# Performance work log

Hardware: AMD Instinct MI355X
Metric: run time of the kernel (lower is better)

## Reference

```python
import jax, jax.numpy as jnp
import numpy as np

H = 64          # hidden_dim
G = 4           # grid_size
NB = 4.0        # neighborhood
PRED = 12       # pred_steps


def _social_pool(all_h, positions, idx, W_sp, b_sp):
    """Vectorized grid-based social pooling. all_h:(N,H), positions:(N,2) -> (H,)."""
    N = positions.shape[0]
    pos_i = positions[idx]
    diff = positions - pos_i                                   # (N,2)
    in_nb = jnp.max(jnp.abs(diff), axis=1) <= NB
    mask = in_nb & (jnp.arange(N) != idx)
    # torch: int(clamp(((d/NB)+1)/2 * G, 0, G-1)); truncation==floor after clip here
    g = jnp.clip(jnp.floor((diff / NB + 1.0) / 2.0 * G), 0, G - 1).astype(jnp.int32)
    cell = g[:, 1] * G + g[:, 0]                               # gy*G + gx, (N,)
    m = mask.astype(all_h.dtype)[:, None]                      # (N,1)
    grid = jax.ops.segment_sum(all_h * m, cell, num_segments=G * G)   # (16,H)
    counts = jax.ops.segment_sum(m, cell, num_segments=G * G)         # (16,1)
    pooled = (grid / jnp.maximum(counts, 1.0)).sum(axis=0)            # (H,)
    return pooled @ W_sp.T + b_sp


def _lstm_cell(inp, h, c, W_ih, b_ih, W_hh, b_hh):
    gates = inp @ W_ih.T + b_ih + h @ W_hh.T + b_hh            # (4H,)
    i, f, g, o = jnp.split(gates, 4)
    i, f, o = jax.nn.sigmoid(i), jax.nn.sigmoid(f), jax.nn.sigmoid(o)
    g = jnp.tanh(g)
    c_new = f * c + i * g
    return o * jnp.tanh(c_new), c_new


def setup_inputs() -> dict:
    key = jax.random.key(0)
    ks = jax.random.split(key, 10)
    N, T = 2_000_000, 8
    s = 0.05
    return {
        "history": jax.random.normal(ks[0], (T, 4), jnp.float32),
        "all_h": jax.random.normal(ks[1], (N, H), jnp.float32),
        "positions": jax.random.normal(ks[2], (N, 2), jnp.float32) * 3.0,
        "W_in": jax.random.normal(ks[3], (H, 4), jnp.float32) * s,
        "b_in": jnp.zeros((H,), jnp.float32),
        "W_ih": jax.random.normal(ks[4], (4 * H, 2 * H), jnp.float32) * s,
        "b_ih": jnp.zeros((4 * H,), jnp.float32),
        "W_hh": jax.random.normal(ks[5], (4 * H, H), jnp.float32) * s,
        "b_hh": jnp.zeros((4 * H,), jnp.float32),
        "W_sp": jax.random.normal(ks[6], (H, H), jnp.float32) * s,
        "b_sp": jnp.zeros((H,), jnp.float32),
        "W_out": jax.random.normal(ks[7], (2, H), jnp.float32) * s,
        "b_out": jnp.zeros((2,), jnp.float32),
        "idx": 0,
    }


def reference(history, all_h, positions, W_in, b_in, W_ih, b_ih, W_hh, b_hh,
              W_sp, b_sp, W_out, b_out, idx):
    # all_h, positions, idx are fixed inputs, so the social vector is identical
    # at every timestep (same math as recomputing it each step in the original).
    social = _social_pool(all_h, positions, idx, W_sp, b_sp)   # (H,)

    def enc_step(carry, x):
        h, c = carry
        emb = x @ W_in.T + b_in
        inp = jnp.concatenate([emb, social])
        h, c = _lstm_cell(inp, h, c, W_ih, b_ih, W_hh, b_hh)
        return (h, c), None

    h0 = jnp.zeros((H,), history.dtype)
    (h, c), _ = jax.lax.scan(enc_step, (h0, h0), history)

    last_pos = history[-1, :2]

    def pred_step(carry, _):
        h, c, lp = carry
        delta = h @ W_out.T + b_out                            # (2,)
        vel = delta / 0.5
        x = jnp.concatenate([lp + delta, vel])                 # (4,)
        emb = x @ W_in.T + b_in
        inp = jnp.concatenate([emb, social])
        h, c = _lstm_cell(inp, h, c, W_ih, b_ih, W_hh, b_hh)
        return (h, c, lp + delta), delta

    _, preds = jax.lax.scan(pred_step, (h, c, last_pos), None, length=PRED)
    return preds  # (pred_steps, 2)
```

## Files before the change

kernel.cpp:

```cpp
#include <hip/hip_runtime.h>

#define HDIM 64
#define CELLS 16
#define WPB 4
#define PV (CELLS * HDIM + CELLS)

__global__ void __launch_bounds__(256) k_pool(
    const float* __restrict__ all_h, const float2* __restrict__ pos2,
    const int* __restrict__ idxp, float* __restrict__ partial,
    int N, int nwaves)
{
    __shared__ float acc[WPB][CELLS * HDIM];
    __shared__ float cnt[WPB][CELLS];
    __shared__ __align__(16) int lst[WPB][64];
    const int tid  = threadIdx.x;
    const int wave = tid >> 6;
    const int lane = tid & 63;

    for (int v = tid; v < WPB * CELLS * HDIM; v += 256) ((float*)acc)[v] = 0.0f;
    if (tid < WPB * CELLS) ((float*)cnt)[tid] = 0.0f;
    __syncthreads();

    const int    idx0 = idxp[0];
    const float2 p0   = pos2[idx0];
    const int    gw   = blockIdx.x * WPB + wave;
    float* __restrict__ accw = acc[wave];
    int*   __restrict__ lstw = lst[wave];

    for (int base = gw * 64; base < N; base += nwaves * 64) {
        const int a = base + lane;
        int cellid = -1;
        if (a < N && a != idx0) {
            const float2 p = pos2[a];
            const float dx = p.x - p0.x;
            const float dy = p.y - p0.y;
            if (fmaxf(fabsf(dx), fabsf(dy)) <= 4.0f) {
                const float f0 = floorf((dx / 4.0f + 1.0f) / 2.0f * 4.0f);
                const float f1 = floorf((dy / 4.0f + 1.0f) / 2.0f * 4.0f);
                const int g0 = (int)fminf(fmaxf(f0, 0.0f), 3.0f);
                const int g1 = (int)fminf(fmaxf(f1, 0.0f), 3.0f);
                cellid = g1 * 4 + g0;
                atomicAdd(&cnt[wave][cellid], 1.0f);
            }
        }
        const unsigned long long mask  = __ballot(cellid >= 0);
        const int                M     = __popcll(mask);
        const unsigned long long below = mask & ((1ULL << lane) - 1ULL);
        if (cellid >= 0) lstw[__popcll(below)] = (lane << 4) | cellid;

        const float* __restrict__ rowp = all_h + (size_t)base * HDIM + lane;
        int r = 0;
        for (; r + 8 <= M; r += 8) {
            const int4 e0 = *(const int4*)&lstw[r];
            const int4 e1 = *(const int4*)&lstw[r + 4];
            const float v0 = rowp[(size_t)(e0.x >> 4) * HDIM];
            const float v1 = rowp[(size_t)(e0.y >> 4) * HDIM];
            const float v2 = rowp[(size_t)(e0.z >> 4) * HDIM];
            const float v3 = rowp[(size_t)(e0.w >> 4) * HDIM];
            const float v4 = rowp[(size_t)(e1.x >> 4) * HDIM];
            const float v5 = rowp[(size_t)(e1.y >> 4) * HDIM];
            const float v6 = rowp[(size_t)(e1.z >> 4) * HDIM];
            const float v7 = rowp[(size_t)(e1.w >> 4) * HDIM];
            accw[(e0.x & 15) * HDIM + lane] += v0;
            accw[(e0.y & 15) * HDIM + lane] += v1;
            accw[(e0.z & 15) * HDIM + lane] += v2;
            accw[(e0.w & 15) * HDIM + lane] += v3;
            accw[(e1.x & 15) * HDIM + lane] += v4;
            accw[(e1.y & 15) * HDIM + lane] += v5;
            accw[(e1.z & 15) * HDIM + lane] += v6;
            accw[(e1.w & 15) * HDIM + lane] += v7;
        }
        for (; r < M; ++r) {
            const int e = lstw[r];
            accw[(e & 15) * HDIM + lane] += rowp[(size_t)(e >> 4) * HDIM];
        }
    }
    __syncthreads();

    float* __restrict__ outp = partial + (size_t)blockIdx.x * PV;
    for (int v = tid; v < CELLS * HDIM; v += 256)
        outp[v] = acc[0][v] + acc[1][v] + acc[2][v] + acc[3][v];
    if (tid < CELLS)
        outp[CELLS * HDIM + tid] = cnt[0][tid] + cnt[1][tid] + cnt[2][tid] + cnt[3][tid];
}

__global__ void __launch_bounds__(256) k_reduce(
    const float* __restrict__ partial, float* __restrict__ finalv, int nbp)
{
    const int wave = threadIdx.x >> 6;
    const int lane = threadIdx.x & 63;
    const int v = blockIdx.x * 4 + wave;
    if (v >= PV) return;
    float s = 0.0f;
    for (int b = lane; b < nbp; b += 64)
        s += partial[(size_t)b * PV + v];
    #pragma unroll
    for (int off = 32; off > 0; off >>= 1)
        s += __shfl_xor(s, off);
    if (lane == 0) finalv[v] = s;
}

__global__ void __launch_bounds__(256) k_lstm(
    const float* __restrict__ finalv, const float* __restrict__ history,
    const float* __restrict__ W_in, const float* __restrict__ b_in,
    const float* __restrict__ W_ih, const float* __restrict__ b_ih,
    const float* __restrict__ W_hh, const float* __restrict__ b_hh,
    const float* __restrict__ W_sp, const float* __restrict__ b_sp,
    const float* __restrict__ W_out, const float* __restrict__ b_out,
    float* __restrict__ out)
{
    __shared__ __align__(16) float pooled[64];
    __shared__ __align__(16) float social[64];
    __shared__ __align__(16) float hl[64];
    __shared__ __align__(16) float cl[64];
    __shared__ float gl[256];
    __shared__ float xs[4];
    __shared__ float lp[2];
    __shared__ float dl[2];
    const int tid = threadIdx.x;

    if (tid < 64) {
        float p = 0.0f;
        #pragma unroll
        for (int c = 0; c < CELLS; ++c) {
            const float cc = finalv[CELLS * HDIM + c];
            p += finalv[c * HDIM + tid] / fmaxf(cc, 1.0f);
        }
        pooled[tid] = p;
    }
    __syncthreads();
    if (tid < 64) {
        float s = b_sp[tid];
        for (int k = 0; k < 64; k += 4) {
            const float4 w4 = *(const float4*)&W_sp[tid * 64 + k];
            s += pooled[k] * w4.x + pooled[k + 1] * w4.y
               + pooled[k + 2] * w4.z + pooled[k + 3] * w4.w;
        }
        social[tid] = s;
        hl[tid] = 0.0f;
        cl[tid] = 0.0f;
    }
    if (tid < 2) lp[tid] = history[7 * 4 + tid];
    __syncthreads();

    float m1k[4] = {0.0f, 0.0f, 0.0f, 0.0f};
    float gconst = b_ih[tid] + b_hh[tid];
    for (int m = 0; m < 64; m += 4) {
        const float4 w4 = *(const float4*)&W_ih[tid * 128 + m];
        const float4 a0 = *(const float4*)&W_in[m * 4];
        const float4 a1 = *(const float4*)&W_in[(m + 1) * 4];
        const float4 a2 = *(const float4*)&W_in[(m + 2) * 4];
        const float4 a3 = *(const float4*)&W_in[(m + 3) * 4];
        m1k[0] += w4.x * a0.x + w4.y * a1.x + w4.z * a2.x + w4.w * a3.x;
        m1k[1] += w4.x * a0.y + w4.y * a1.y + w4.z * a2.y + w4.w * a3.y;
        m1k[2] += w4.x * a0.z + w4.y * a1.z + w4.z * a2.z + w4.w * a3.z;
        m1k[3] += w4.x * a0.w + w4.y * a1.w + w4.z * a2.w + w4.w * a3.w;
        gconst += w4.x * b_in[m] + w4.y * b_in[m + 1]
                + w4.z * b_in[m + 2] + w4.w * b_in[m + 3];
    }
    for (int k = 0; k < 64; k += 4) {
        const float4 w4 = *(const float4*)&W_ih[tid * 128 + 64 + k];
        gconst += w4.x * social[k] + w4.y * social[k + 1]
                + w4.z * social[k + 2] + w4.w * social[k + 3];
    }
    float whh[64];
    #pragma unroll
    for (int k = 0; k < 64; k += 4) {
        const float4 w4 = *(const float4*)&W_hh[tid * 64 + k];
        whh[k] = w4.x; whh[k + 1] = w4.y; whh[k + 2] = w4.z; whh[k + 3] = w4.w;
    }

    for (int t = 0; t < 8; ++t) {
        __syncthreads();
        if (tid < 4) xs[tid] = history[t * 4 + tid];
        __syncthreads();
        float g0 = gconst + m1k[0] * xs[0] + m1k[1] * xs[1];
        float g1 = m1k[2] * xs[2] + m1k[3] * xs[3];
        float g2 = 0.0f, g3 = 0.0f;
        #pragma unroll
        for (int k = 0; k < 64; k += 16) {
            const float4 a = *(const float4*)&hl[k];
            const float4 b = *(const float4*)&hl[k + 4];
            const float4 c = *(const float4*)&hl[k + 8];
            const float4 d = *(const float4*)&hl[k + 12];
            g0 += whh[k] * a.x + whh[k + 1] * a.y + whh[k + 2] * a.z + whh[k + 3] * a.w;
            g1 += whh[k + 4] * b.x + whh[k + 5] * b.y + whh[k + 6] * b.z + whh[k + 7] * b.w;
            g2 += whh[k + 8] * c.x + whh[k + 9] * c.y + whh[k + 10] * c.z + whh[k + 11] * c.w;
            g3 += whh[k + 12] * d.x + whh[k + 13] * d.y + whh[k + 14] * d.z + whh[k + 15] * d.w;
        }
        gl[tid] = (g0 + g1) + (g2 + g3);
        __syncthreads();
        if (tid < 64) {
            const float ig = 1.0f / (1.0f + expf(-gl[tid]));
            const float fg = 1.0f / (1.0f + expf(-gl[64 + tid]));
            const float gg = tanhf(gl[128 + tid]);
            const float og = 1.0f / (1.0f + expf(-gl[192 + tid]));
            const float cn = fg * cl[tid] + ig * gg;
            cl[tid] = cn;
            hl[tid] = og * tanhf(cn);
        }
    }

    for (int t = 0; t < 12; ++t) {
        __syncthreads();
        if (tid < 2) {
            float d = b_out[tid];
            for (int k = 0; k < 64; k += 4) {
                const float4 w4 = *(const float4*)&W_out[tid * 64 + k];
                d += w4.x * hl[k] + w4.y * hl[k + 1] + w4.z * hl[k + 2] + w4.w * hl[k + 3];
            }
            dl[tid] = d;
            out[t * 2 + tid] = d;
        }
        __syncthreads();
        if (tid < 2) {
            const float npos = lp[tid] + dl[tid];
            xs[tid] = npos;
            xs[2 + tid] = dl[tid] * 2.0f;
            lp[tid] = npos;
        }
        __syncthreads();
        float g0 = gconst + m1k[0] * xs[0] + m1k[1] * xs[1];
        float g1 = m1k[2] * xs[2] + m1k[3] * xs[3];
        float g2 = 0.0f, g3 = 0.0f;
        #pragma unroll
        for (int k = 0; k < 64; k += 16) {
            const float4 a = *(const float4*)&hl[k];
            const float4 b = *(const float4*)&hl[k + 4];
            const float4 c = *(const float4*)&hl[k + 8];
            const float4 d = *(const float4*)&hl[k + 12];
            g0 += whh[k] * a.x + whh[k + 1] * a.y + whh[k + 2] * a.z + whh[k + 3] * a.w;
            g1 += whh[k + 4] * b.x + whh[k + 5] * b.y + whh[k + 6] * b.z + whh[k + 7] * b.w;
            g2 += whh[k + 8] * c.x + whh[k + 9] * c.y + whh[k + 10] * c.z + whh[k + 11] * c.w;
            g3 += whh[k + 12] * d.x + whh[k + 13] * d.y + whh[k + 14] * d.z + whh[k + 15] * d.w;
        }
        gl[tid] = (g0 + g1) + (g2 + g3);
        __syncthreads();
        if (tid < 64) {
            const float ig = 1.0f / (1.0f + expf(-gl[tid]));
            const float fg = 1.0f / (1.0f + expf(-gl[64 + tid]));
            const float gg = tanhf(gl[128 + tid]);
            const float og = 1.0f / (1.0f + expf(-gl[192 + tid]));
            const float cn = fg * cl[tid] + ig * gg;
            cl[tid] = cn;
            hl[tid] = og * tanhf(cn);
        }
    }
}

extern "C" void kernel_launch(void* const* d_in, const int* in_sizes, int n_in,
                              void* d_out, int out_size, void* d_ws, size_t ws_size,
                              hipStream_t stream) {
    const float* history   = (const float*)d_in[0];
    const float* all_h     = (const float*)d_in[1];
    const float* positions = (const float*)d_in[2];
    const float* W_in  = (const float*)d_in[3];
    const float* b_in  = (const float*)d_in[4];
    const float* W_ih  = (const float*)d_in[5];
    const float* b_ih  = (const float*)d_in[6];
    const float* W_hh  = (const float*)d_in[7];
    const float* b_hh  = (const float*)d_in[8];
    const float* W_sp  = (const float*)d_in[9];
    const float* b_sp  = (const float*)d_in[10];
    const float* W_out = (const float*)d_in[11];
    const float* b_out = (const float*)d_in[12];
    const int*   idxp  = (const int*)d_in[13];
    const int N = in_sizes[2] / 2;

    float* ws      = (float*)d_ws;
    float* finalv  = ws;
    float* partial = ws + PV;

    long long avail = (long long)(ws_size / sizeof(float)) - PV;
    int nbp = 2048;
    if ((long long)nbp * PV > avail) nbp = (int)(avail / PV);
    if (nbp < 1) nbp = 1;

    k_pool<<<nbp, 256, 0, stream>>>(all_h, (const float2*)positions, idxp,
                                    partial, N, nbp * WPB);
    k_reduce<<<(PV + 3) / 4, 256, 0, stream>>>(partial, finalv, nbp);
    k_lstm<<<1, 256, 0, stream>>>(finalv, history, W_in, b_in, W_ih, b_ih,
                                  W_hh, b_hh, W_sp, b_sp, W_out, b_out,
                                  (float*)d_out);
}
```

Baseline: 75.75 us.

## Precompute LSTM input constants in reduce kernel, warm caches, trim LSTM syncs

An extra block is added to the reduce kernel. It precomputes the input-projection folding (W_ih times W_in, plus the bias constant) into workspace, and touches the W_ih, W_hh, W_sp and W_out weights to warm the cache ahead of the serial LSTM kernel. The LSTM kernel now caches history in shared memory and computes the output projection with a wave shuffle reduction instead of two threads. This removes two barriers per prediction step. The pooling gather loop also gains a 16-wide unrolled stage to raise memory-level parallelism, at the cost of more registers.

```diff
diff --git a/kernel.cpp b/kernel.cpp
--- a/kernel.cpp
+++ b/kernel.cpp
@@ -4,6 +4,11 @@
 #define CELLS 16
 #define WPB 4
 #define PV (CELLS * HDIM + CELLS)
+
+#define WS_M1K   1040
+#define WS_G0    2064
+#define WS_SINK  2320
+#define WS_PART  2576
 
 __global__ void __launch_bounds__(256) k_pool(
     const float* __restrict__ all_h, const float2* __restrict__ pos2,
@@ -50,6 +55,44 @@
 
         const float* __restrict__ rowp = all_h + (size_t)base * HDIM + lane;
         int r = 0;
+        for (; r + 16 <= M; r += 16) {
+            const int4 e0 = *(const int4*)&lstw[r];
+            const int4 e1 = *(const int4*)&lstw[r + 4];
+            const int4 e2 = *(const int4*)&lstw[r + 8];
+            const int4 e3 = *(const int4*)&lstw[r + 12];
+            const float v0  = rowp[(size_t)(e0.x >> 4) * HDIM];
+            const float v1  = rowp[(size_t)(e0.y >> 4) * HDIM];
+            const float v2  = rowp[(size_t)(e0.z >> 4) * HDIM];
+            const float v3  = rowp[(size_t)(e0.w >> 4) * HDIM];
+            const float v4  = rowp[(size_t)(e1.x >> 4) * HDIM];
+            const float v5  = rowp[(size_t)(e1.y >> 4) * HDIM];
+            const float v6  = rowp[(size_t)(e1.z >> 4) * HDIM];
+            const float v7  = rowp[(size_t)(e1.w >> 4) * HDIM];
+            const float v8  = rowp[(size_t)(e2.x >> 4) * HDIM];
+            const float v9  = rowp[(size_t)(e2.y >> 4) * HDIM];
+            const float v10 = rowp[(size_t)(e2.z >> 4) * HDIM];
+            const float v11 = rowp[(size_t)(e2.w >> 4) * HDIM];
+            const float v12 = rowp[(size_t)(e3.x >> 4) * HDIM];
+            const float v13 = rowp[(size_t)(e3.y >> 4) * HDIM];
+            const float v14 = rowp[(size_t)(e3.z >> 4) * HDIM];
+            const float v15 = rowp[(size_t)(e3.w >> 4) * HDIM];
+            accw[(e0.x & 15) * HDIM + lane] += v0;
+            accw[(e0.y & 15) * HDIM + lane] += v1;
+            accw[(e0.z & 15) * HDIM + lane] += v2;
+            accw[(e0.w & 15) * HDIM + lane] += v3;
+            accw[(e1.x & 15) * HDIM + lane] += v4;
+            accw[(e1.y & 15) * HDIM + lane] += v5;
+            accw[(e1.z & 15) * HDIM + lane] += v6;
+            accw[(e1.w & 15) * HDIM + lane] += v7;
+            accw[(e2.x & 15) * HDIM + lane] += v8;
+            accw[(e2.y & 15) * HDIM + lane] += v9;
+            accw[(e2.z & 15) * HDIM + lane] += v10;
+            accw[(e2.w & 15) * HDIM + lane] += v11;
+            accw[(e3.x & 15) * HDIM + lane] += v12;
+            accw[(e3.y & 15) * HDIM + lane] += v13;
+            accw[(e3.z & 15) * HDIM + lane] += v14;
+            accw[(e3.w & 15) * HDIM + lane] += v15;
+        }
         for (; r + 8 <= M; r += 8) {
             const int4 e0 = *(const int4*)&lstw[r];
             const int4 e1 = *(const int4*)&lstw[r + 4];
@@ -85,26 +128,63 @@
 }
 
 __global__ void __launch_bounds__(256) k_reduce(
-    const float* __restrict__ partial, float* __restrict__ finalv, int nbp)
-{
-    const int wave = threadIdx.x >> 6;
-    const int lane = threadIdx.x & 63;
-    const int v = blockIdx.x * 4 + wave;
-    if (v >= PV) return;
-    float s = 0.0f;
-    for (int b = lane; b < nbp; b += 64)
-        s += partial[(size_t)b * PV + v];
-    #pragma unroll
-    for (int off = 32; off > 0; off >>= 1)
-        s += __shfl_xor(s, off);
-    if (lane == 0) finalv[v] = s;
-}
-
-__global__ void __launch_bounds__(256) k_lstm(
-    const float* __restrict__ finalv, const float* __restrict__ history,
+    const float* __restrict__ partial, float* __restrict__ ws,
     const float* __restrict__ W_in, const float* __restrict__ b_in,
     const float* __restrict__ W_ih, const float* __restrict__ b_ih,
     const float* __restrict__ W_hh, const float* __restrict__ b_hh,
+    const float* __restrict__ W_sp, const float* __restrict__ W_out,
+    int nbp)
+{
+    const int tid = threadIdx.x;
+    if (blockIdx.x < 260) {
+        const int wave = tid >> 6;
+        const int lane = tid & 63;
+        const int v = blockIdx.x * 4 + wave;
+        if (v >= PV) return;
+        float s = 0.0f;
+        for (int b = lane; b < nbp; b += 64)
+            s += partial[(size_t)b * PV + v];
+        #pragma unroll
+        for (int off = 32; off > 0; off >>= 1)
+            s += __shfl_xor(s, off);
+        if (lane == 0) ws[v] = s;
+        return;
+    }
+    float m0 = 0.0f, m1 = 0.0f, m2 = 0.0f, m3 = 0.0f;
+    float gc = b_ih[tid] + b_hh[tid];
+    for (int m = 0; m < 64; m += 4) {
+        const float4 w4 = *(const float4*)&W_ih[tid * 128 + m];
+        const float4 a0 = *(const float4*)&W_in[m * 4];
+        const float4 a1 = *(const float4*)&W_in[(m + 1) * 4];
+        const float4 a2 = *(const float4*)&W_in[(m + 2) * 4];
+        const float4 a3 = *(const float4*)&W_in[(m + 3) * 4];
+        m0 += w4.x * a0.x + w4.y * a1.x + w4.z * a2.x + w4.w * a3.x;
+        m1 += w4.x * a0.y + w4.y * a1.y + w4.z * a2.y + w4.w * a3.y;
+        m2 += w4.x * a0.z + w4.y * a1.z + w4.z * a2.z + w4.w * a3.z;
+        m3 += w4.x * a0.w + w4.y * a1.w + w4.z * a2.w + w4.w * a3.w;
+        gc += w4.x * b_in[m] + w4.y * b_in[m + 1]
+            + w4.z * b_in[m + 2] + w4.w * b_in[m + 3];
+    }
+    float4 mv; mv.x = m0; mv.y = m1; mv.z = m2; mv.w = m3;
+    *(float4*)&ws[WS_M1K + tid * 4] = mv;
+    ws[WS_G0 + tid] = gc;
+    float warm = 0.0f;
+    for (int k = 0; k < 64; k += 4) {
+        const float4 a = *(const float4*)&W_ih[tid * 128 + 64 + k];
+        const float4 b = *(const float4*)&W_hh[tid * 64 + k];
+        warm += a.x + a.y + a.z + a.w + b.x + b.y + b.z + b.w;
+    }
+    for (int k = 0; k < 16; k += 4) {
+        const float4 c = *(const float4*)&W_sp[tid * 16 + k];
+        warm += c.x + c.y + c.z + c.w;
+    }
+    warm += W_out[tid & 127];
+    ws[WS_SINK + tid] = warm;
+}
+
+__global__ void __launch_bounds__(256) k_lstm(
+    const float* __restrict__ ws, const float* __restrict__ history,
+    const float* __restrict__ W_ih, const float* __restrict__ W_hh,
     const float* __restrict__ W_sp, const float* __restrict__ b_sp,
     const float* __restrict__ W_out, const float* __restrict__ b_out,
     float* __restrict__ out)
@@ -114,17 +194,18 @@
     __shared__ __align__(16) float hl[64];
     __shared__ __align__(16) float cl[64];
     __shared__ float gl[256];
+    __shared__ __align__(16) float histl[32];
     __shared__ float xs[4];
     __shared__ float lp[2];
-    __shared__ float dl[2];
     const int tid = threadIdx.x;
 
+    if (tid < 32) histl[tid] = history[tid];
     if (tid < 64) {
         float p = 0.0f;
         #pragma unroll
         for (int c = 0; c < CELLS; ++c) {
-            const float cc = finalv[CELLS * HDIM + c];
-            p += finalv[c * HDIM + tid] / fmaxf(cc, 1.0f);
+            const float cc = ws[CELLS * HDIM + c];
+            p += ws[c * HDIM + tid] / fmaxf(cc, 1.0f);
         }
         pooled[tid] = p;
     }
@@ -140,24 +221,11 @@
         hl[tid] = 0.0f;
         cl[tid] = 0.0f;
     }
-    if (tid < 2) lp[tid] = history[7 * 4 + tid];
-    __syncthreads();
-
-    float m1k[4] = {0.0f, 0.0f, 0.0f, 0.0f};
-    float gconst = b_ih[tid] + b_hh[tid];
-    for (int m = 0; m < 64; m += 4) {
-        const float4 w4 = *(const float4*)&W_ih[tid * 128 + m];
-        const float4 a0 = *(const float4*)&W_in[m * 4];
-        const float4 a1 = *(const float4*)&W_in[(m + 1) * 4];
-        const float4 a2 = *(const float4*)&W_in[(m + 2) * 4];
-        const float4 a3 = *(const float4*)&W_in[(m + 3) * 4];
-        m1k[0] += w4.x * a0.x + w4.y * a1.x + w4.z * a2.x + w4.w * a3.x;
-        m1k[1] += w4.x * a0.y + w4.y * a1.y + w4.z * a2.y + w4.w * a3.y;
-        m1k[2] += w4.x * a0.z + w4.y * a1.z + w4.z * a2.z + w4.w * a3.z;
-        m1k[3] += w4.x * a0.w + w4.y * a1.w + w4.z * a2.w + w4.w * a3.w;
-        gconst += w4.x * b_in[m] + w4.y * b_in[m + 1]
-                + w4.z * b_in[m + 2] + w4.w * b_in[m + 3];
-    }
+    if (tid == 0) { lp[0] = histl[28]; lp[1] = histl[29]; }
+    __syncthreads();
+
+    const float4 mv = *(const float4*)&ws[WS_M1K + tid * 4];
+    float gconst = ws[WS_G0 + tid];
     for (int k = 0; k < 64; k += 4) {
         const float4 w4 = *(const float4*)&W_ih[tid * 128 + 64 + k];
         gconst += w4.x * social[k] + w4.y * social[k + 1]
@@ -169,13 +237,18 @@
         const float4 w4 = *(const float4*)&W_hh[tid * 64 + k];
         whh[k] = w4.x; whh[k + 1] = w4.y; whh[k + 2] = w4.z; whh[k + 3] = w4.w;
     }
+    float wout0 = 0.0f, wout1 = 0.0f, bo0 = 0.0f, bo1 = 0.0f;
+    if (tid < 64) {
+        wout0 = W_out[tid]; wout1 = W_out[64 + tid];
+        bo0 = b_out[0]; bo1 = b_out[1];
+    }
+    __syncthreads();
 
     for (int t = 0; t < 8; ++t) {
-        __syncthreads();
-        if (tid < 4) xs[tid] = history[t * 4 + tid];
-        __syncthreads();
-        float g0 = gconst + m1k[0] * xs[0] + m1k[1] * xs[1];
-        float g1 = m1k[2] * xs[2] + m1k[3] * xs[3];
+        const float x0 = histl[t * 4 + 0], x1 = histl[t * 4 + 1];
+        const float x2 = histl[t * 4 + 2], x3 = histl[t * 4 + 3];
+        float g0 = gconst + mv.x * x0 + mv.y * x1;
+        float g1 = mv.z * x2 + mv.w * x3;
         float g2 = 0.0f, g3 = 0.0f;
         #pragma unroll
         for (int k = 0; k < 64; k += 16) {
@@ -199,29 +272,32 @@
             cl[tid] = cn;
             hl[tid] = og * tanhf(cn);
         }
+        __syncthreads();
     }
 
     for (int t = 0; t < 12; ++t) {
-        __syncthreads();
-        if (tid < 2) {
-            float d = b_out[tid];
-            for (int k = 0; k < 64; k += 4) {
-                const float4 w4 = *(const float4*)&W_out[tid * 64 + k];
-                d += w4.x * hl[k] + w4.y * hl[k + 1] + w4.z * hl[k + 2] + w4.w * hl[k + 3];
+        if (tid < 64) {
+            float s0 = wout0 * hl[tid];
+            float s1 = wout1 * hl[tid];
+            #pragma unroll
+            for (int off = 32; off > 0; off >>= 1) {
+                s0 += __shfl_xor(s0, off);
+                s1 += __shfl_xor(s1, off);
             }
-            dl[tid] = d;
-            out[t * 2 + tid] = d;
-        }
-        __syncthreads();
-        if (tid < 2) {
-            const float npos = lp[tid] + dl[tid];
-            xs[tid] = npos;
-            xs[2 + tid] = dl[tid] * 2.0f;
-            lp[tid] = npos;
-        }
-        __syncthreads();
-        float g0 = gconst + m1k[0] * xs[0] + m1k[1] * xs[1];
-        float g1 = m1k[2] * xs[2] + m1k[3] * xs[3];
+            if (tid == 0) {
+                const float d0 = s0 + bo0, d1 = s1 + bo1;
+                out[t * 2 + 0] = d0;
+                out[t * 2 + 1] = d1;
+                const float n0 = lp[0] + d0, n1 = lp[1] + d1;
+                xs[0] = n0; xs[1] = n1;
+                xs[2] = d0 * 2.0f; xs[3] = d1 * 2.0f;
+                lp[0] = n0; lp[1] = n1;
+            }
+        }
+        __syncthreads();
+        const float x0 = xs[0], x1 = xs[1], x2 = xs[2], x3 = xs[3];
+        float g0 = gconst + mv.x * x0 + mv.y * x1;
+        float g1 = mv.z * x2 + mv.w * x3;
         float g2 = 0.0f, g3 = 0.0f;
         #pragma unroll
         for (int k = 0; k < 64; k += 16) {
@@ -245,6 +321,7 @@
             cl[tid] = cn;
             hl[tid] = og * tanhf(cn);
         }
+        __syncthreads();
     }
 }
 
@@ -268,18 +345,17 @@
     const int N = in_sizes[2] / 2;
 
     float* ws      = (float*)d_ws;
-    float* finalv  = ws;
-    float* partial = ws + PV;
-
-    long long avail = (long long)(ws_size / sizeof(float)) - PV;
+    float* partial = ws + WS_PART;
+
+    long long avail = (long long)(ws_size / sizeof(float)) - WS_PART;
     int nbp = 2048;
     if ((long long)nbp * PV > avail) nbp = (int)(avail / PV);
     if (nbp < 1) nbp = 1;
 
     k_pool<<<nbp, 256, 0, stream>>>(all_h, (const float2*)positions, idxp,
                                     partial, N, nbp * WPB);
-    k_reduce<<<(PV + 3) / 4, 256, 0, stream>>>(partial, finalv, nbp);
-    k_lstm<<<1, 256, 0, stream>>>(finalv, history, W_in, b_in, W_ih, b_ih,
-                                  W_hh, b_hh, W_sp, b_sp, W_out, b_out,
-                                  (float*)d_out);
+    k_reduce<<<261, 256, 0, stream>>>(partial, ws, W_in, b_in, W_ih, b_ih,
+                                      W_hh, b_hh, W_sp, W_out, nbp);
+    k_lstm<<<1, 256, 0, stream>>>(ws, history, W_ih, W_hh, W_sp, b_sp,
+                                  W_out, b_out, (float*)d_out);
 }
```

New measurement: 74.06 us. 1.02x faster.
